# Performance work log

Measured on AMD Instinct MI355X. Metric: run time of the kernel, lower is better.

Reference implementation:

```python
import jax, jax.numpy as jnp
import numpy as np

B, N, IN_DIM, OUT_DIM = 4, 2048, 1024, 512


def setup_inputs() -> dict:
    key = jax.random.key(0)
    k1, k2, k3, k4, k5 = jax.random.split(key, 5)
    x = jax.random.normal(k1, (B, N, IN_DIM), dtype=jnp.float32)
    fc_w = jax.random.normal(k2, (OUT_DIM, IN_DIM), dtype=jnp.float32) * (1.0 / np.sqrt(IN_DIM))
    fc_b = jax.random.normal(k3, (OUT_DIM,), dtype=jnp.float32) * 0.01
    attn_w = jax.random.normal(k4, (1, 2 * OUT_DIM), dtype=jnp.float32) * (1.0 / np.sqrt(2 * OUT_DIM))
    attn_b = jax.random.normal(k5, (1,), dtype=jnp.float32) * 0.01
    return {"x": x, "fc_w": fc_w, "fc_b": fc_b, "attn_w": attn_w, "attn_b": attn_b}


def reference(x, fc_w, fc_b, attn_w, attn_b):
    # h = fc(x): [B, N, D]
    h = jnp.einsum('bni,di->bnd', x, fc_w) + fc_b
    D = h.shape[-1]
    # attn(cat([h_i, h_j])) == h_i @ a1 + h_j @ a2 + b  (exact factorization of
    # the Linear over the concat axis; avoids the O(N^2 * 2D) concat tensor)
    a1 = attn_w[0, :D]   # weights multiplying h_i
    a2 = attn_w[0, D:]   # weights multiplying h_j
    s1 = h @ a1          # [B, N]
    s2 = h @ a2          # [B, N]
    e = s1[:, :, None] + s2[:, None, :] + attn_b[0]  # [B, N, N]
    alpha = jax.nn.softmax(e, axis=-1)
    out = jnp.einsum('bij,bjd->bid', alpha, h)       # [B, N, D]
    return out
```

## Files before the change

kernel.cpp:

```cpp
#include <hip/hip_runtime.h>

#define BATCH 4
#define NROWS 2048
#define IN_DIM 1024
#define OUT_DIM 512
#define DSPLIT 16
#define NCHUNK 256
#define RPB 32

typedef float f4 __attribute__((ext_vector_type(4)));

__global__ void __launch_bounds__(256)
k1_w2part(const float* __restrict__ fc_w,
          const float* __restrict__ attn_w,
          float* __restrict__ w2part) {
    int ds = blockIdx.x >> 2, cg = blockIdx.x & 3;
    int col = (cg << 8) + threadIdx.x;
    int d0 = ds << 5;
    float acc = 0.f;
#pragma unroll 8
    for (int j = 0; j < 32; ++j)
        acc += fc_w[(size_t)(d0 + j) * IN_DIM + col] * attn_w[OUT_DIM + d0 + j];
    w2part[(ds << 10) + col] = acc;
}

__global__ void __launch_bounds__(512)
k2_chunk(const float* __restrict__ x,
         const float* __restrict__ w2part,
         float* __restrict__ yu,
         float* __restrict__ Zc) {
    const int bid = blockIdx.x, t = threadIdx.x;
    const int w = t >> 6, lane = t & 63;
    __shared__ float w2s[IN_DIM];
    __shared__ f4 sbuf[8 * 256];
    __shared__ float zbuf[8];

    if (t < 256) {
        const f4* wp = (const f4*)w2part;
        f4 s = {0.f, 0.f, 0.f, 0.f};
#pragma unroll
        for (int ds = 0; ds < DSPLIT; ++ds) s += wp[(ds << 8) + t];
        ((f4*)w2s)[t] = s;
    }
    __syncthreads();

    const f4* x4 = (const f4*)x;
    const f4* w2s4 = (const f4*)w2s;
    const f4 u0 = w2s4[lane],       u1 = w2s4[lane + 64],
             u2 = w2s4[lane + 128], u3 = w2s4[lane + 192];

    size_t row0 = (size_t)bid * RPB + (w << 2);
    f4 a0 = {0,0,0,0}, a1 = {0,0,0,0}, a2 = {0,0,0,0}, a3 = {0,0,0,0};
    float zw = 0.f;
#pragma unroll
    for (int r = 0; r < 4; ++r) {
        size_t base = (row0 + r) << 8;
        f4 v0 = __builtin_nontemporal_load(&x4[base + lane]);
        f4 v1 = __builtin_nontemporal_load(&x4[base + lane + 64]);
        f4 v2 = __builtin_nontemporal_load(&x4[base + lane + 128]);
        f4 v3 = __builtin_nontemporal_load(&x4[base + lane + 192]);
        f4 p = v0 * u0 + v1 * u1 + v2 * u2 + v3 * u3;
        float d = (p.x + p.y) + (p.z + p.w);
#pragma unroll
        for (int off = 32; off; off >>= 1) d += __shfl_xor(d, off, 64);
        float e = __expf(d);
        zw += e;
        a0 += e * v0; a1 += e * v1; a2 += e * v2; a3 += e * v3;
    }
    sbuf[(w << 8) + lane]       = a0;
    sbuf[(w << 8) + lane + 64]  = a1;
    sbuf[(w << 8) + lane + 128] = a2;
    sbuf[(w << 8) + lane + 192] = a3;
    if (lane == 0) zbuf[w] = zw;
    __syncthreads();

    {
        const float2* sb2 = (const float2*)sbuf;
        float2 s = {0.f, 0.f};
#pragma unroll
        for (int i = 0; i < 8; ++i) {
            float2 q = sb2[(i << 9) + t];
            s.x += q.x; s.y += q.y;
        }
        ((float2*)(yu + ((size_t)bid << 10)))[t] = s;
    }
    if (t == 0) {
        float z = 0.f;
#pragma unroll
        for (int i = 0; i < 8; ++i) z += zbuf[i];
        Zc[bid] = z;
    }
}

__global__ void __launch_bounds__(256)
k3_yc(const float* __restrict__ yu,
      const float* __restrict__ Zc,
      const float* __restrict__ fc_w,
      const float* __restrict__ fc_b,
      float* __restrict__ cb) {
    const int b = blockIdx.x >> 5, ds = blockIdx.x & 31;
    const int t = threadIdx.x, w = t >> 6, lane = t & 63;
    __shared__ float ys[IN_DIM];
    __shared__ float zsh;

    if (w == 0) {
        float z = Zc[(b << 6) + lane];
#pragma unroll
        for (int off = 32; off; off >>= 1) z += __shfl_xor(z, off, 64);
        if (lane == 0) zsh = 1.f / z;
    }

    const f4* yu4 = (const f4*)yu + ((size_t)b << 14);
    f4 acc = {0.f, 0.f, 0.f, 0.f};
#pragma unroll 8
    for (int c = 0; c < 64; ++c) acc += yu4[(c << 8) + t];
    __syncthreads();
    acc *= zsh;
    ((f4*)ys)[t] = acc;
    __syncthreads();

    const f4* ys4 = (const f4*)ys;
    const f4 y0 = ys4[lane],       y1 = ys4[lane + 64],
             y2 = ys4[lane + 128], y3 = ys4[lane + 192];
#pragma unroll
    for (int q = 0; q < 4; ++q) {
        int d = (ds << 4) + (w << 2) + q;
        const f4* fr = (const f4*)fc_w + ((size_t)d << 8);
        f4 p = fr[lane] * y0 + fr[lane + 64] * y1 + fr[lane + 128] * y2 + fr[lane + 192] * y3;
        float s = (p.x + p.y) + (p.z + p.w);
#pragma unroll
        for (int off = 32; off; off >>= 1) s += __shfl_xor(s, off, 64);
        if (lane == 0) cb[(b << 9) + d] = s + fc_b[d];
    }
}

__global__ void __launch_bounds__(256)
k4_bcast(const float* __restrict__ cb, f4* __restrict__ out) {
    const int bid = blockIdx.x, t = threadIdx.x;
    const int row0 = bid << 2;
    const int b = row0 >> 11;
    __shared__ f4 cs[128];
    if (t < 128) cs[t] = ((const f4*)cb)[(b << 7) + t];
    __syncthreads();
    f4* o = out + ((size_t)row0 << 7);
    f4 v = cs[t & 127];
    __builtin_nontemporal_store(v, o + t);
    __builtin_nontemporal_store(v, o + t + 256);
}

extern "C" void kernel_launch(void* const* d_in, const int* in_sizes, int n_in,
                              void* d_out, int out_size, void* d_ws, size_t ws_size,
                              hipStream_t stream) {
    const float* x      = (const float*)d_in[0];
    const float* fc_w   = (const float*)d_in[1];
    const float* fc_b   = (const float*)d_in[2];
    const float* attn_w = (const float*)d_in[3];

    float* wsf    = (float*)d_ws;
    float* w2part = wsf;
    float* Zc     = w2part + DSPLIT * IN_DIM;
    float* yu     = Zc + NCHUNK;
    float* cb     = yu + (size_t)NCHUNK * IN_DIM;
    float* out    = (float*)d_out;

    k1_w2part<<<64,     256, 0, stream>>>(fc_w, attn_w, w2part);
    k2_chunk <<<NCHUNK, 512, 0, stream>>>(x, w2part, yu, Zc);
    k3_yc    <<<128,    256, 0, stream>>>(yu, Zc, fc_w, fc_b, cb);
    k4_bcast <<<2048,   256, 0, stream>>>(cb, (f4*)out);
}
```

Before: 29.02 us.

## Fuse output-vector computation with broadcast store into a single kernel

After: 29.05 us. About the same (+0.1%).

```diff
diff --git a/kernel.cpp b/kernel.cpp
--- a/kernel.cpp
+++ b/kernel.cpp
@@ -93,14 +93,16 @@
 }
 
 __global__ void __launch_bounds__(256)
-k3_yc(const float* __restrict__ yu,
-      const float* __restrict__ Zc,
-      const float* __restrict__ fc_w,
-      const float* __restrict__ fc_b,
-      float* __restrict__ cb) {
-    const int b = blockIdx.x >> 5, ds = blockIdx.x & 31;
+k3_fused(const float* __restrict__ yu,
+         const float* __restrict__ Zc,
+         const float* __restrict__ fc_w,
+         const float* __restrict__ fc_b,
+         f4* __restrict__ out) {
+    const int bid = blockIdx.x;
+    const int b = bid >> 5, rem = bid & 31, ds = rem >> 1, rg = rem & 1;
     const int t = threadIdx.x, w = t >> 6, lane = t & 63;
     __shared__ float ys[IN_DIM];
+    __shared__ float cs[32];
     __shared__ float zsh;
 
     if (w == 0) {
@@ -123,29 +125,24 @@
     const f4 y0 = ys4[lane],       y1 = ys4[lane + 64],
              y2 = ys4[lane + 128], y3 = ys4[lane + 192];
 #pragma unroll
-    for (int q = 0; q < 4; ++q) {
-        int d = (ds << 4) + (w << 2) + q;
+    for (int q = 0; q < 8; ++q) {
+        int dl = (w << 3) + q;
+        int d = (ds << 5) + dl;
         const f4* fr = (const f4*)fc_w + ((size_t)d << 8);
         f4 p = fr[lane] * y0 + fr[lane + 64] * y1 + fr[lane + 128] * y2 + fr[lane + 192] * y3;
         float s = (p.x + p.y) + (p.z + p.w);
 #pragma unroll
         for (int off = 32; off; off >>= 1) s += __shfl_xor(s, off, 64);
-        if (lane == 0) cb[(b << 9) + d] = s + fc_b[d];
+        if (lane == 0) cs[dl] = s + fc_b[d];
     }
-}
+    __syncthreads();
 
-__global__ void __launch_bounds__(256)
-k4_bcast(const float* __restrict__ cb, f4* __restrict__ out) {
-    const int bid = blockIdx.x, t = threadIdx.x;
-    const int row0 = bid << 2;
-    const int b = row0 >> 11;
-    __shared__ f4 cs[128];
-    if (t < 128) cs[t] = ((const f4*)cb)[(b << 7) + t];
-    __syncthreads();
-    f4* o = out + ((size_t)row0 << 7);
-    f4 v = cs[t & 127];
-    __builtin_nontemporal_store(v, o + t);
-    __builtin_nontemporal_store(v, o + t + 256);
+    const f4 val = ((const f4*)cs)[t & 7];
+    const int lr = t >> 3;
+    size_t base = ((size_t)b * NROWS + ((size_t)rg << 10) + lr) * 128 + (ds << 3) + (t & 7);
+#pragma unroll
+    for (int it = 0; it < 32; ++it)
+        __builtin_nontemporal_store(val, out + base + (size_t)it * 32 * 128);
 }
 
 extern "C" void kernel_launch(void* const* d_in, const int* in_sizes, int n_in,
@@ -160,11 +157,9 @@
     float* w2part = wsf;
     float* Zc     = w2part + DSPLIT * IN_DIM;
     float* yu     = Zc + NCHUNK;
-    float* cb     = yu + (size_t)NCHUNK * IN_DIM;
     float* out    = (float*)d_out;
 
     k1_w2part<<<64,     256, 0, stream>>>(fc_w, attn_w, w2part);
     k2_chunk <<<NCHUNK, 512, 0, stream>>>(x, w2part, yu, Zc);
-    k3_yc    <<<128,    256, 0, stream>>>(yu, Zc, fc_w, fc_b, cb);
-    k4_bcast <<<2048,   256, 0, stream>>>(cb, (f4*)out);
+    k3_fused <<<128,    256, 0, stream>>>(yu, Zc, fc_w, fc_b, (f4*)out);
 }
```
